# Kernel tuning notes

Hardware: AMD Instinct MI355X
Metric: run time of the kernel (lower is better)

## Reference

```python
import jax, jax.numpy as jnp
import numpy as np

LAYERS = 10
EPS = 1e-08


def setup_inputs() -> dict:
    key = jax.random.key(0)
    # [B, agents, N, N] assignment logits; row 0 along dim 2 is the depot row
    output = jax.random.normal(key, (32, 8, 512, 512), dtype=jnp.float32)
    return {"output": output}


def reference(output):
    # Max-subtraction for numerical stability before exp.
    # Depot row: max over dim 3 only. Other rows: max over dims (1, 3).
    if LAYERS > 0:
        depots_max = jnp.max(output[:, :, :1, :], axis=3, keepdims=True)
        others_max = jnp.max(output[:, :, 1:, :], axis=(1, 3), keepdims=True)
        output = jnp.concatenate(
            [output[:, :, :1, :] - depots_max,
             output[:, :, 1:, :] - others_max],
            axis=2,
        )
    output = jnp.exp(output)
    # Sinkhorn-style alternating normalization; transpose(2,3) each iter
    # alternates which axis gets normalized.
    for _ in range(LAYERS):
        output = jnp.maximum(output, EPS)
        starts = output[:, :, :1, :]
        starts = starts / jnp.sum(starts, axis=3, keepdims=True)
        nexts = output[:, :, 1:, :]
        nexts = nexts / jnp.sum(nexts, axis=(1, 3), keepdims=True)
        output = jnp.concatenate([starts, nexts], axis=2)
        output = jnp.swapaxes(output, 2, 3)
    if LAYERS % 2 != 0:
        output = jnp.swapaxes(output, 2, 3)
    return output
```

## Files before the change

### kernel.cpp

```cpp
#include <hip/hip_runtime.h>
#include <hip/hip_cooperative_groups.h>
#include <math.h>

#define B 32
#define H 8
#define N 512
#define NBLK 256
#define TPB 512
#define RPB 64
#define OFF_E0   8388608
#define OFF_EC   (OFF_E0 + 131072)
#define OFF_PA   (OFF_EC + 131072)
#define OFF_PB   (OFF_PA + 131072)
#define OFF_C0A  (OFF_PB + 131072)
#define OFF_C0B  (OFF_C0A + 2048)

typedef float f32x4 __attribute__((ext_vector_type(4)));

__device__ __forceinline__ float atomLoad(const float* p) {
    return __hip_atomic_load(p, __ATOMIC_RELAXED, __HIP_MEMORY_SCOPE_AGENT);
}
__device__ __forceinline__ void atomStore(float* p, float v) {
    __hip_atomic_store(p, v, __ATOMIC_RELAXED, __HIP_MEMORY_SCOPE_AGENT);
}

__device__ __forceinline__ void group_barrier(int* cnt, int target) {
    __syncthreads();
    if (threadIdx.x == 0) {
        __hip_atomic_fetch_add(cnt, 1, __ATOMIC_RELAXED, __HIP_MEMORY_SCOPE_AGENT);
        while (__hip_atomic_load(cnt, __ATOMIC_RELAXED, __HIP_MEMORY_SCOPE_AGENT) < target)
            __builtin_amdgcn_s_sleep(2);
    }
    __syncthreads();
}

__global__ __launch_bounds__(128) void k_build(const float* __restrict__ in,
                                               float* __restrict__ G,
                                               float* __restrict__ E0,
                                               float* __restrict__ Ec) {
    const int i = blockIdx.x;
    const int b = blockIdx.y;
    const int t = threadIdx.x;
    const size_t inb = (size_t)b * H * N * N;
    float4 acc = make_float4(0.f, 0.f, 0.f, 0.f);
#pragma unroll
    for (int h = 0; h < H; ++h) {
        const float4 x = *reinterpret_cast<const float4*>(
            in + inb + ((size_t)h * N + i) * N + t * 4);
        float4 e;
        e.x = __expf(x.x); e.y = __expf(x.y); e.z = __expf(x.z); e.w = __expf(x.w);
        acc.x += e.x; acc.y += e.y; acc.z += e.z; acc.w += e.w;
        if (t == 0) Ec[(b * H + h) * N + i] = e.x;
        if (i == 0) *reinterpret_cast<float4*>(E0 + (b * H + h) * N + t * 4) = e;
    }
    *reinterpret_cast<float4*>(G + ((size_t)b * N + i) * N + t * 4) = acc;
}

__global__ __launch_bounds__(TPB) void k_coop(const float* __restrict__ G,
                                              const float* __restrict__ E0,
                                              const float* __restrict__ Ec,
                                              float* __restrict__ partA,
                                              float* __restrict__ partB,
                                              float* __restrict__ c0pA,
                                              float* __restrict__ c0pB,
                                              float* __restrict__ rv,
                                              float* __restrict__ r0v,
                                              float* __restrict__ cv,
                                              float* __restrict__ c0v,
                                              int* __restrict__ counters) {
    __shared__ float Gs[RPB][N];
    __shared__ float E0g[N];
    __shared__ float vec[N];
    __shared__ float EcS[H][RPB];
    __shared__ float rloc[RPB];
    __shared__ float c0rec[H];
    __shared__ float r0loc_s;

    const int blk = blockIdx.x;
    const int b = blk >> 3;
    const int g = blk & 7;
    const int rbase = g * RPB;
    const bool owner = (g == 0);
    const int tid = threadIdx.x;
    const int w = tid >> 6, lane = tid & 63;
    int* cnt = counters + b * 16;

    {
        const float4* Gg = reinterpret_cast<const float4*>(G + ((size_t)(b * N) + rbase) * N);
        float4* Gl = reinterpret_cast<float4*>(&Gs[0][0]);
#pragma unroll
        for (int k = 0; k < RPB * N / 4 / TPB; ++k) {
            const int t = k * TPB + tid;
            __builtin_amdgcn_global_load_lds(
                (const __attribute__((address_space(1))) void*)(Gg + t),
                (__attribute__((address_space(3))) void*)(Gl + t),
                16, 0, 0);
        }
    }
    for (int t = tid; t < H * RPB; t += TPB)
        EcS[t / RPB][t % RPB] = Ec[(b * H + (t / RPB)) * N + rbase + (t % RPB)];
    E0g[tid] = E0[(b * H + g) * N + tid];
    const float E00g = Ec[(b * H + g) * N];
    __syncthreads();

    for (int it = 0; it < 5; ++it) {
        if (it == 0) {
            vec[tid] = (tid == 0) ? 0.0f : 1.0f;
            if (tid < H) c0rec[tid] = 1.0f;
        } else {
            const float* pr = (it & 1) ? partB : partA;
            pr += (size_t)b * 8 * N;
            float cs = 0.0f;
#pragma unroll
            for (int gg = 0; gg < 8; ++gg) cs += atomLoad(&pr[gg * N + tid]);
            vec[tid] = (tid == 0) ? 0.0f : 1.0f / cs;
            if (tid < H) {
                const float* qr = (it & 1) ? c0pB : c0pA;
                qr += b * 8 * H;
                float s = 0.0f;
#pragma unroll
                for (int gg = 0; gg < 8; ++gg) s += atomLoad(&qr[gg * H + tid]);
                c0rec[tid] = 1.0f / s;
            }
        }
        __syncthreads();
        float cj[8];
#pragma unroll
        for (int k = 0; k < 8; ++k) cj[k] = vec[lane + 64 * k];
#pragma unroll
        for (int r8 = 0; r8 < 8; ++r8) {
            const int il = w * 8 + r8;
            float pacc = 0.0f;
#pragma unroll
            for (int k = 0; k < 8; ++k) pacc += Gs[il][lane + 64 * k] * cj[k];
#pragma unroll
            for (int s = 32; s > 0; s >>= 1) pacc += __shfl_down(pacc, s, 64);
            if (lane == 0) {
                float s2 = pacc;
#pragma unroll
                for (int h = 0; h < H; ++h) s2 += EcS[h][il] * c0rec[h];
                float rva = 1.0f / s2;
                rloc[il] = rva;
                if (it == 4) rv[b * N + rbase + il] = rva;
            }
        }
        if (w == g) {
            float pacc = 0.0f;
#pragma unroll
            for (int k = 0; k < 8; ++k) pacc += E0g[lane + 64 * k] * cj[k];
#pragma unroll
            for (int s = 32; s > 0; s >>= 1) pacc += __shfl_down(pacc, s, 64);
            if (lane == 0) {
                float v = 1.0f / (pacc + E00g * c0rec[g]);
                r0loc_s = v;
                if (it == 4) r0v[b * H + g] = v;
            }
        }
        __syncthreads();
        {
            float* pw = ((it + 1) & 1) ? partB : partA;
            float* qw = ((it + 1) & 1) ? c0pB : c0pA;
            const float r0l = r0loc_s;
            float acc = 0.0f;
            const int il0 = owner ? 1 : 0;
#pragma unroll 8
            for (int il = il0; il < RPB; ++il) acc += Gs[il][tid] * rloc[il];
            acc += E0g[tid] * r0l;
            atomStore(&pw[((size_t)(b * 8) + g) * N + tid], acc);
            float q = EcS[w][lane] * ((owner && lane == 0) ? 0.0f : rloc[lane]);
            if (w == g && lane == 0) q += E00g * r0l;
#pragma unroll
            for (int s = 32; s > 0; s >>= 1) q += __shfl_down(q, s, 64);
            if (lane == 0) atomStore(&qw[(b * 8 + g) * H + w], q);
        }
        group_barrier(cnt, (it + 1) * 8);
    }
    if (owner) {
        const float* pr = partB + (size_t)b * 8 * N;
        float cs = 0.0f;
#pragma unroll
        for (int gg = 0; gg < 8; ++gg) cs += atomLoad(&pr[gg * N + tid]);
        cv[b * N + tid] = (tid == 0) ? 1.0f : 1.0f / cs;
        if (tid < H) {
            const float* qr = c0pB + b * 8 * H;
            float s = 0.0f;
#pragma unroll
            for (int gg = 0; gg < 8; ++gg) s += atomLoad(&qr[gg * H + tid]);
            c0v[b * H + tid] = 1.0f / s;
        }
    }
}

__global__ __launch_bounds__(256) void k_final(const float* __restrict__ in,
                                               const float* __restrict__ rv,
                                               const float* __restrict__ r0v,
                                               const float* __restrict__ cv,
                                               const float* __restrict__ c0v,
                                               float* __restrict__ out) {
    const size_t v0 = (size_t)blockIdx.x * 1024 + threadIdx.x;
#pragma unroll
    for (int s = 0; s < 4; ++s) {
        const size_t v = v0 + (size_t)s * 256;
        const int j4 = (int)(v & 127);
        size_t rest = v >> 7;
        const int i = (int)(rest & 511); rest >>= 9;
        const int h = (int)(rest & 7);
        const int b = (int)(rest >> 3);
        const float R = (i == 0) ? r0v[b * H + h] : rv[b * N + i];
        const f32x4 x = __builtin_nontemporal_load(reinterpret_cast<const f32x4*>(in) + v);
        float4 cl = reinterpret_cast<const float4*>(cv + b * N)[j4];
        if (j4 == 0) cl.x = c0v[b * H + h];
        f32x4 o;
        o.x = __expf(x.x) * R * cl.x;
        o.y = __expf(x.y) * R * cl.y;
        o.z = __expf(x.z) * R * cl.z;
        o.w = __expf(x.w) * R * cl.w;
        __builtin_nontemporal_store(o, reinterpret_cast<f32x4*>(out) + v);
    }
}

extern "C" void kernel_launch(void* const* d_in, const int* in_sizes, int n_in,
                              void* d_out, int out_size, void* d_ws, size_t ws_size,
                              hipStream_t stream) {
    (void)in_sizes; (void)n_in; (void)out_size; (void)ws_size;
    const float* in = (const float*)d_in[0];
    float* out = (float*)d_out;
    float* ws = (float*)d_ws;

    float* rv  = ws;
    float* cv  = ws + 16384;
    float* r0v = ws + 32768;
    float* c0v = ws + 33024;
    int* counters = (int*)(ws + 33280);

    float* G   = out;
    float* E0  = out + OFF_E0;
    float* Ec  = out + OFF_EC;
    float* pA  = out + OFF_PA;
    float* pB  = out + OFF_PB;
    float* c0A = out + OFF_C0A;
    float* c0B = out + OFF_C0B;

    hipMemsetAsync(counters, 0, B * 16 * sizeof(int), stream);

    k_build<<<dim3(N, B), 128, 0, stream>>>(in, G, E0, Ec);

    void* args[] = {(void*)&G, (void*)&E0, (void*)&Ec, (void*)&pA, (void*)&pB,
                    (void*)&c0A, (void*)&c0B, (void*)&rv, (void*)&r0v,
                    (void*)&cv, (void*)&c0v, (void*)&counters};
    hipLaunchCooperativeKernel(reinterpret_cast<void*>(k_coop), dim3(NBLK), dim3(TPB),
                               args, 0, stream);

    k_final<<<16384, 256, 0, stream>>>(in, rv, r0v, cv, c0v, out);
}
```

Baseline: 211.8 us.

## Double cooperative block threads, split column partials in halves, fold counter reset into build

Raises the cooperative kernel's block size from 512 to 1024 threads. Each wave now handles 4 rows instead of 8 in the row pass, and the column-partial pass is split into two halves of 32 rows, with the partial buffers doubled to 16 slices per batch. It also drops the separate memset launch by zeroing the barrier counters inside the build kernel, and switches the build kernel's input reads to nontemporal loads. The goal is more parallelism in the serial Sinkhorn iterations and one fewer launch. In exchange the readers must sum more partials, and register pressure rises at 1024 threads.

```diff
diff --git a/kernel.cpp b/kernel.cpp
--- a/kernel.cpp
+++ b/kernel.cpp
@@ -6,13 +6,13 @@
 #define H 8
 #define N 512
 #define NBLK 256
-#define TPB 512
+#define TPB 1024
 #define RPB 64
 #define OFF_E0   8388608
 #define OFF_EC   (OFF_E0 + 131072)
 #define OFF_PA   (OFF_EC + 131072)
-#define OFF_PB   (OFF_PA + 131072)
-#define OFF_C0A  (OFF_PB + 131072)
+#define OFF_PB   (OFF_PA + 262144)
+#define OFF_C0A  (OFF_PB + 262144)
 #define OFF_C0B  (OFF_C0A + 2048)
 
 typedef float f32x4 __attribute__((ext_vector_type(4)));
@@ -37,16 +37,21 @@
 __global__ __launch_bounds__(128) void k_build(const float* __restrict__ in,
                                                float* __restrict__ G,
                                                float* __restrict__ E0,
-                                               float* __restrict__ Ec) {
+                                               float* __restrict__ Ec,
+                                               int* __restrict__ counters) {
     const int i = blockIdx.x;
     const int b = blockIdx.y;
     const int t = threadIdx.x;
+    if (i == 0 && b == 0) {
+#pragma unroll
+        for (int k = 0; k < 4; ++k) counters[k * 128 + t] = 0;
+    }
     const size_t inb = (size_t)b * H * N * N;
     float4 acc = make_float4(0.f, 0.f, 0.f, 0.f);
 #pragma unroll
     for (int h = 0; h < H; ++h) {
-        const float4 x = *reinterpret_cast<const float4*>(
-            in + inb + ((size_t)h * N + i) * N + t * 4);
+        const f32x4 x = __builtin_nontemporal_load(
+            reinterpret_cast<const f32x4*>(in + inb + ((size_t)h * N + i) * N) + t);
         float4 e;
         e.x = __expf(x.x); e.y = __expf(x.y); e.z = __expf(x.z); e.w = __expf(x.w);
         acc.x += e.x; acc.y += e.y; acc.z += e.z; acc.w += e.w;
@@ -97,23 +102,25 @@
                 16, 0, 0);
         }
     }
-    for (int t = tid; t < H * RPB; t += TPB)
-        EcS[t / RPB][t % RPB] = Ec[(b * H + (t / RPB)) * N + rbase + (t % RPB)];
-    E0g[tid] = E0[(b * H + g) * N + tid];
+    if (tid < H * RPB)
+        EcS[tid >> 6][tid & 63] = Ec[(b * H + (tid >> 6)) * N + rbase + (tid & 63)];
+    if (tid < N) E0g[tid] = E0[(b * H + g) * N + tid];
     const float E00g = Ec[(b * H + g) * N];
     __syncthreads();
 
     for (int it = 0; it < 5; ++it) {
         if (it == 0) {
-            vec[tid] = (tid == 0) ? 0.0f : 1.0f;
+            if (tid < N) vec[tid] = (tid == 0) ? 0.0f : 1.0f;
             if (tid < H) c0rec[tid] = 1.0f;
         } else {
-            const float* pr = (it & 1) ? partB : partA;
-            pr += (size_t)b * 8 * N;
-            float cs = 0.0f;
-#pragma unroll
-            for (int gg = 0; gg < 8; ++gg) cs += atomLoad(&pr[gg * N + tid]);
-            vec[tid] = (tid == 0) ? 0.0f : 1.0f / cs;
+            if (tid < N) {
+                const float* pr = (it & 1) ? partB : partA;
+                pr += (size_t)b * 16 * N;
+                float cs = 0.0f;
+#pragma unroll
+                for (int gg = 0; gg < 16; ++gg) cs += atomLoad(&pr[gg * N + tid]);
+                vec[tid] = (tid == 0) ? 0.0f : 1.0f / cs;
+            }
             if (tid < H) {
                 const float* qr = (it & 1) ? c0pB : c0pA;
                 qr += b * 8 * H;
@@ -128,8 +135,8 @@
 #pragma unroll
         for (int k = 0; k < 8; ++k) cj[k] = vec[lane + 64 * k];
 #pragma unroll
-        for (int r8 = 0; r8 < 8; ++r8) {
-            const int il = w * 8 + r8;
+        for (int r4 = 0; r4 < 4; ++r4) {
+            const int il = (w << 2) | r4;
             float pacc = 0.0f;
 #pragma unroll
             for (int k = 0; k < 8; ++k) pacc += Gs[il][lane + 64 * k] * cj[k];
@@ -161,26 +168,33 @@
             float* pw = ((it + 1) & 1) ? partB : partA;
             float* qw = ((it + 1) & 1) ? c0pB : c0pA;
             const float r0l = r0loc_s;
+            const int j = tid & 511;
+            const int half = tid >> 9;
+            const int beg = half * 32 + ((owner && half == 0) ? 1 : 0);
+            const int end = half * 32 + 32;
             float acc = 0.0f;
-            const int il0 = owner ? 1 : 0;
 #pragma unroll 8
-            for (int il = il0; il < RPB; ++il) acc += Gs[il][tid] * rloc[il];
-            acc += E0g[tid] * r0l;
-            atomStore(&pw[((size_t)(b * 8) + g) * N + tid], acc);
-            float q = EcS[w][lane] * ((owner && lane == 0) ? 0.0f : rloc[lane]);
-            if (w == g && lane == 0) q += E00g * r0l;
-#pragma unroll
-            for (int s = 32; s > 0; s >>= 1) q += __shfl_down(q, s, 64);
-            if (lane == 0) atomStore(&qw[(b * 8 + g) * H + w], q);
+            for (int il = beg; il < end; ++il) acc += Gs[il][j] * rloc[il];
+            if (half == 0) acc += E0g[j] * r0l;
+            atomStore(&pw[((size_t)(b * 16) + (g * 2 + half)) * N + j], acc);
+            if (w < 8) {
+                float q = EcS[w][lane] * ((owner && lane == 0) ? 0.0f : rloc[lane]);
+                if (w == g && lane == 0) q += E00g * r0l;
+#pragma unroll
+                for (int s = 32; s > 0; s >>= 1) q += __shfl_down(q, s, 64);
+                if (lane == 0) atomStore(&qw[(b * 8 + g) * H + w], q);
+            }
         }
         group_barrier(cnt, (it + 1) * 8);
     }
     if (owner) {
-        const float* pr = partB + (size_t)b * 8 * N;
-        float cs = 0.0f;
-#pragma unroll
-        for (int gg = 0; gg < 8; ++gg) cs += atomLoad(&pr[gg * N + tid]);
-        cv[b * N + tid] = (tid == 0) ? 1.0f : 1.0f / cs;
+        if (tid < N) {
+            const float* pr = partB + (size_t)b * 16 * N;
+            float cs = 0.0f;
+#pragma unroll
+            for (int gg = 0; gg < 16; ++gg) cs += atomLoad(&pr[gg * N + tid]);
+            cv[b * N + tid] = (tid == 0) ? 1.0f : 1.0f / cs;
+        }
         if (tid < H) {
             const float* qr = c0pB + b * 8 * H;
             float s = 0.0f;
@@ -241,9 +255,7 @@
     float* c0A = out + OFF_C0A;
     float* c0B = out + OFF_C0B;
 
-    hipMemsetAsync(counters, 0, B * 16 * sizeof(int), stream);
-
-    k_build<<<dim3(N, B), 128, 0, stream>>>(in, G, E0, Ec);
+    k_build<<<dim3(N, B), 128, 0, stream>>>(in, G, E0, Ec, counters);
 
     void* args[] = {(void*)&G, (void*)&E0, (void*)&Ec, (void*)&pA, (void*)&pB,
                     (void*)&c0A, (void*)&c0B, (void*)&rv, (void*)&r0v,
```

Measured after the change: 212.3 us. Within noise of the previous version (+0.3%).
